# Performance work log

Measured on AMD Instinct MI355X. Metric: run time of the kernel, lower is better.

Reference implementation:

```python
import jax, jax.numpy as jnp
import numpy as np

BN_EPS = 1e-5

def conv2d(x, w, pad):
    return jax.lax.conv_general_dilated(x, w, (1, 1), [(pad, pad), (pad, pad)],
                                        dimension_numbers=('NCHW', 'OIHW', 'NCHW'))

def bn(x, g, b, m, v):
    # eval-mode batchnorm with running stats
    c = (None, slice(None), None, None)
    return g[c] * (x - m[c]) * jax.lax.rsqrt(v[c] + BN_EPS) + b[c]

def criss_cross_attention(x, wq, wk, wv, gamma):
    # x: (B, C, H, W); q/k have reduced dim d = C//8
    B, C, H, W = x.shape
    q = jnp.einsum('bchw,dc->bdhw', x, wq)
    k = jnp.einsum('bchw,dc->bdhw', x, wk)
    v = jnp.einsum('bchw,dc->bdhw', x, wv)
    # column (vertical) affinities: for each (h,w), keys at (k,w) -> (B,H,W,H)
    eH = jnp.einsum('bdhw,bdkw->bhwk', q, k)
    # -inf on the h==k diagonal (avoid counting the center pixel twice)
    eH = eH + jnp.where(jnp.eye(H, dtype=bool), -jnp.inf, 0.0)[None, :, None, :]
    # row (horizontal) affinities: keys at (h,k) -> (B,H,W,W)
    eW = jnp.einsum('bdhw,bdhk->bhwk', q, k)
    att = jax.nn.softmax(jnp.concatenate([eH, eW], axis=3), axis=3)  # (B,H,W,H+W)
    aH, aW = att[..., :H], att[..., H:]
    oH = jnp.einsum('bhwk,bdkw->bdhw', aH, v)
    oW = jnp.einsum('bhwk,bdhk->bdhw', aW, v)
    return gamma * (oH + oW) + x

def upsample_bilinear_align_corners(x, out_h, out_w):
    # torch nn.Upsample(mode='bilinear', align_corners=True)
    def interp(x, size, axis):
        n = x.shape[axis]
        pos = jnp.arange(size, dtype=x.dtype) * ((n - 1) / (size - 1))
        lo = jnp.floor(pos).astype(jnp.int32)
        hi = jnp.minimum(lo + 1, n - 1)
        w = pos - lo.astype(x.dtype)
        shp = [1] * x.ndim; shp[axis] = size
        w = w.reshape(shp)
        return jnp.take(x, lo, axis=axis) * (1 - w) + jnp.take(x, hi, axis=axis) * w
    x = interp(x, out_h, 2)
    return interp(x, out_w, 3)

def setup_inputs() -> dict:
    key = jax.random.key(0)
    ks = jax.random.split(key, 16)
    B, C, H, W = 2, 2048, 96, 96
    ic = C // 32          # inter_c = 64
    dq = ic // 8          # 8
    nc = 19
    s = 0.05
    return {
        'x': jax.random.normal(ks[0], (B, C, H, W), jnp.float32),
        'w_in': jax.random.normal(ks[1], (ic, C, 3, 3), jnp.float32) * s,
        'bn_in_g': jnp.ones((ic,), jnp.float32),
        'bn_in_b': jnp.zeros((ic,), jnp.float32),
        'bn_in_m': jax.random.normal(ks[2], (ic,), jnp.float32) * 0.1,
        'bn_in_v': jax.random.uniform(ks[3], (ic,), jnp.float32, 0.5, 1.5),
        'wq': jax.random.normal(ks[4], (dq, ic), jnp.float32) * s,
        'wk': jax.random.normal(ks[5], (dq, ic), jnp.float32) * s,
        'wv': jax.random.normal(ks[6], (ic, ic), jnp.float32) * s,
        'cca_gamma': jax.random.uniform(ks[7], (1,), jnp.float32, 0.2, 0.8),
        'w_out': jax.random.normal(ks[8], (ic, ic, 3, 3), jnp.float32) * s,
        'bn_out_g': jnp.ones((ic,), jnp.float32),
        'bn_out_b': jnp.zeros((ic,), jnp.float32),
        'bn_out_m': jax.random.normal(ks[9], (ic,), jnp.float32) * 0.1,
        'bn_out_v': jax.random.uniform(ks[10], (ic,), jnp.float32, 0.5, 1.5),
        'w_cls1': jax.random.normal(ks[11], (ic, C + ic, 3, 3), jnp.float32) * s,
        'bn_cls_g': jnp.ones((ic,), jnp.float32),
        'bn_cls_b': jnp.zeros((ic,), jnp.float32),
        'bn_cls_m': jax.random.normal(ks[12], (ic,), jnp.float32) * 0.1,
        'bn_cls_v': jax.random.uniform(ks[13], (ic,), jnp.float32, 0.5, 1.5),
        'w_cls2': jax.random.normal(ks[14], (nc, ic, 1, 1), jnp.float32) * s,
    }

def reference(x, w_in, bn_in_g, bn_in_b, bn_in_m, bn_in_v,
              wq, wk, wv, cca_gamma,
              w_out, bn_out_g, bn_out_b, bn_out_m, bn_out_v,
              w_cls1, bn_cls_g, bn_cls_b, bn_cls_m, bn_cls_v, w_cls2):
    RECURRENCE = 2
    out = jax.nn.relu(bn(conv2d(x, w_in, 1), bn_in_g, bn_in_b, bn_in_m, bn_in_v))
    for _ in range(RECURRENCE):
        out = criss_cross_attention(out, wq, wk, wv, cca_gamma)
    out = jax.nn.relu(bn(conv2d(out, w_out, 1), bn_out_g, bn_out_b, bn_out_m, bn_out_v))
    out = jnp.concatenate([x, out], axis=1)
    # cls_seg: conv -> BN (no relu) -> upsample x8 (bilinear, align_corners) -> 1x1 conv
    out = bn(conv2d(out, w_cls1, 1), bn_cls_g, bn_cls_b, bn_cls_m, bn_cls_v)
    H, W = out.shape[2], out.shape[3]
    out = upsample_bilinear_align_corners(out, H * 8, W * 8)
    out = conv2d(out, w_cls2, 0)
    return out
```

## Files before the change

### kernel.cpp

```cpp
#include <hip/hip_runtime.h>
#include <stdint.h>

#define HW 9216

typedef float f32x4 __attribute__((ext_vector_type(4)));
typedef short s16x8 __attribute__((ext_vector_type(8)));

#define PIN() asm volatile("" ::: "memory")
#define WAITV12() asm volatile("s_waitcnt vmcnt(12)" ::: "memory")

__device__ __forceinline__ unsigned short f2bf(float f){
  union { float fv; uint32_t u; } x; x.fv = f;
  uint32_t u = x.u;
  u += 0x7fffu + ((u >> 16) & 1u);
  return (unsigned short)(u >> 16);
}
__device__ __forceinline__ float bf2f(unsigned short s){
  union { uint32_t u; float fv; } x; x.u = ((uint32_t)s) << 16;
  return x.fv;
}

__device__ __forceinline__ void gload16(const void* g, void* l){
  __builtin_amdgcn_global_load_lds(
    (const __attribute__((address_space(1))) unsigned int*)g,
    (__attribute__((address_space(3))) unsigned int*)l, 16, 0, 0);
}

__global__ __launch_bounds__(256) void transp_pack_kernel(const float* __restrict__ x,
    unsigned short* __restrict__ xT,
    const float* __restrict__ w_in, const float* __restrict__ w_out,
    const float* __restrict__ w_cls1, unsigned short* __restrict__ WpIn,
    unsigned short* __restrict__ WpOut, unsigned short* __restrict__ WpCls,
    unsigned short* __restrict__ zp){
  __shared__ unsigned short tl[256 * 66];
  int blk = blockIdx.x;
  int tid = threadIdx.x;
  if (blk < 2304){
    int b = blk / 1152; int r = blk - b * 1152;
    int cchunk = r / 144, pxt = r - cchunk * 144;
    int c0 = cchunk * 256, px0 = pxt * 64;
    for (int e = tid; e < 4096; e += 256){
      int cc = e >> 4, pq = e & 15;
      float4 v4 = *(const float4*)(x + ((size_t)(b * 2048 + c0 + cc)) * HW + px0 + pq * 4);
      const float* vp = (const float*)&v4;
      #pragma unroll
      for (int j = 0; j < 4; j++) tl[cc * 66 + pq * 4 + j] = f2bf(vp[j]);
    }
    __syncthreads();
    for (int j = tid; j < 2048; j += 256){
      int px = j >> 5, oct = j & 31;
      s16x8 pk;
      #pragma unroll
      for (int t = 0; t < 8; t++) pk[t] = (short)tl[(oct * 8 + t) * 66 + px];
      *(s16x8*)(xT + ((size_t)(b * 9216 + px0 + px)) * 2048 + c0 + oct * 8) = pk;
    }
  } else {
    if (blk == 2304 && tid < 64) ((unsigned int*)zp)[tid] = 0u;
    const int N0 = 64 * 2048 * 9, N1 = 64 * 64 * 9, N2 = 64 * 2112 * 9;
    int total = N0 + N1 + N2;
    int nblk = gridDim.x - 2304;
    for (int i = (blk - 2304) * 256 + tid; i < total; i += nblk * 256){
      const float* w; unsigned short* Wp; int Cin; int idx;
      if (i < N0){ w = w_in; Wp = WpIn; Cin = 2048; idx = i; }
      else if (i < N0 + N1){ w = w_out; Wp = WpOut; Cin = 64; idx = i - N0; }
      else { w = w_cls1; Wp = WpCls; Cin = 2112; idx = i - N0 - N1; }
      int c = idx & 31; int r = idx >> 5; int o = r & 63; int r2 = r >> 6;
      int tap = r2 % 9; int ck = r2 / 9;
      Wp[idx] = f2bf(w[((size_t)o * Cin + ck * 32 + c) * 9 + tap]);
    }
  }
}

template<int T>
__device__ __forceinline__ void tapbody(const char* hb, s16x8 (&bs)[4], f32x4 (&acc)[4][4],
    const unsigned short* wbase, int gmax, int g0, int wv, int ln, int kg){
  constexpr int dy = T / 3, dx = T - dy * 3;
  #pragma unroll
  for (int mf = 0; mf < 4; mf++){
    int p = (wv * 4 + mf + dy) * 18 + (ln + dx);
    int aoff = p * 64 + ((kg ^ (p & 3)) << 4);
    s16x8 a = *(const s16x8*)(hb + aoff);
    #pragma unroll
    for (int nf = 0; nf < 4; nf++)
      acc[mf][nf] = __builtin_amdgcn_mfma_f32_16x16x32_bf16(a, bs[nf], acc[mf][nf], 0, 0, 0);
  }
  constexpr int dck = (T + 3) / 9, dt = (T + 3) % 9;
  if (g0 + T + 3 < gmax){
    const unsigned short* wb2 = wbase + dck * 18432 + dt * 2048;
    #pragma unroll
    for (int nf = 0; nf < 4; nf++) bs[nf] = *(const s16x8*)(wb2 + nf * 512);
  }
}

__global__ __launch_bounds__(256, 2) void conv_nhwc_kernel(
    const unsigned short* __restrict__ A0, int c0stride,
    const unsigned short* __restrict__ A1, int nck0,
    const unsigned short* __restrict__ Wp,
    unsigned short* __restrict__ sl, int nchunks,
    const unsigned short* __restrict__ zp){
  int mt = blockIdx.x;
  int b = mt / 36; int r = mt - b * 36;
  int h0 = (r / 6) * 16, w0 = (r % 6) * 16;
  int KS = gridDim.y, ks = blockIdx.y;
  int c0 = (nchunks * ks) / KS, c1 = (nchunks * (ks + 1)) / KS;
  int tid = threadIdx.x, lane = tid & 63, wv = tid >> 6;
  int ln = lane & 15, kg = lane >> 4;
  __shared__ char halo[2][24576];

  int pixb0[6], pixb1[6]; bool val[6];
  #pragma unroll
  for (int rr = 0; rr < 6; rr++){
    int i = tid + rr * 256;
    int p = i >> 2, q_lds = i & 3;
    int logq = q_lds ^ (p & 3);
    int hh = p / 18, ww = p - hh * 18;
    int h = h0 - 1 + hh, w = w0 - 1 + ww;
    bool v = (i < 1296) && ((unsigned)h < 96u) && ((unsigned)w < 96u);
    val[rr] = v;
    int pix = (b * 96 + h) * 96 + w;
    pixb0[rr] = v ? (pix * c0stride * 2 + logq * 16) : 0;
    pixb1[rr] = v ? (pix * 128 + logq * 16) : 0;
  }
  const char* a0B = (const char*)A0;
  const char* a1B = (const char*)A1;
  const char* zpB = (const char*)zp;

  auto stage = [&](char* ldsB, int ck){
    bool inA0 = (ck < nck0);
    int chb0 = ck * 64, chb1 = (ck - nck0) * 64;
    #pragma unroll
    for (int rr = 0; rr < 6; rr++){
      const char* src = zpB;
      if (val[rr]) src = inA0 ? (a0B + pixb0[rr] + chb0) : (a1B + pixb1[rr] + chb1);
      gload16(src, ldsB + (tid + rr * 256) * 16);
    }
  };

  f32x4 acc[4][4];
  #pragma unroll
  for (int i = 0; i < 4; i++)
    #pragma unroll
    for (int j = 0; j < 4; j++) acc[i][j] = (f32x4)(0.f);

  s16x8 bs0[4], bs1[4], bs2[4];
  int gmax = (c1 - c0) * 9;

  stage(&halo[0][0], c0);
  PIN();
  {
    const unsigned short* w0b = Wp + (size_t)c0 * 18432 + ln * 32 + kg * 8;
    #pragma unroll
    for (int nf = 0; nf < 4; nf++){
      bs0[nf] = *(const s16x8*)(w0b + 0 * 2048 + nf * 512);
      bs1[nf] = *(const s16x8*)(w0b + 1 * 2048 + nf * 512);
      bs2[nf] = *(const s16x8*)(w0b + 2 * 2048 + nf * 512);
    }
  }
  WAITV12();
  __builtin_amdgcn_s_barrier();

  for (int ck = c0; ck < c1; ck++){
    int cur = (ck - c0) & 1;
    if (ck + 1 < c1){ stage(&halo[cur ^ 1][0], ck + 1); PIN(); }
    const unsigned short* wbase = Wp + (size_t)ck * 18432 + ln * 32 + kg * 8;
    const char* hb = &halo[cur][0];
    int g0 = (ck - c0) * 9;
    tapbody<0>(hb, bs0, acc, wbase, gmax, g0, wv, ln, kg);
    tapbody<1>(hb, bs1, acc, wbase, gmax, g0, wv, ln, kg);
    tapbody<2>(hb, bs2, acc, wbase, gmax, g0, wv, ln, kg);
    tapbody<3>(hb, bs0, acc, wbase, gmax, g0, wv, ln, kg);
    tapbody<4>(hb, bs1, acc, wbase, gmax, g0, wv, ln, kg);
    tapbody<5>(hb, bs2, acc, wbase, gmax, g0, wv, ln, kg);
    tapbody<6>(hb, bs0, acc, wbase, gmax, g0, wv, ln, kg);
    tapbody<7>(hb, bs1, acc, wbase, gmax, g0, wv, ln, kg);
    tapbody<8>(hb, bs2, acc, wbase, gmax, g0, wv, ln, kg);
    if (ck + 1 < c1){
      WAITV12();
      __builtin_amdgcn_s_barrier();
    }
  }

  unsigned short* base = sl + ((size_t)(ks * 72 + mt)) * 16384;
  #pragma unroll
  for (int mf = 0; mf < 4; mf++)
    #pragma unroll
    for (int nf = 0; nf < 4; nf++){
      int o = nf * 16 + ln;
      #pragma unroll
      for (int rr = 0; rr < 4; rr++){
        int m = wv * 64 + mf * 16 + kg * 4 + rr;
        base[m * 64 + o] = f2bf(acc[mf][nf][rr]);
      }
    }
}

__global__ __launch_bounds__(256, 2) void conv_out_kernel(
    const unsigned short* __restrict__ A0,
    const unsigned short* __restrict__ Wp,
    const float* __restrict__ g, const float* __restrict__ bb,
    const float* __restrict__ mm, const float* __restrict__ vv,
    unsigned short* __restrict__ outT,
    const unsigned short* __restrict__ zp){
  int mt = blockIdx.x;
  int b = mt / 36; int r = mt - b * 36;
  int h0 = (r / 6) * 16, w0 = (r % 6) * 16;
  int tid = threadIdx.x, lane = tid & 63, wv = tid >> 6;
  int ln = lane & 15, kg = lane >> 4;
  __shared__ char halo[2][24576];

  int pixb0[6]; bool val[6];
  #pragma unroll
  for (int rr = 0; rr < 6; rr++){
    int i = tid + rr * 256;
    int p = i >> 2, q_lds = i & 3;
    int logq = q_lds ^ (p & 3);
    int hh = p / 18, ww = p - hh * 18;
    int h = h0 - 1 + hh, w = w0 - 1 + ww;
    bool v = (i < 1296) && ((unsigned)h < 96u) && ((unsigned)w < 96u);
    val[rr] = v;
    int pix = (b * 96 + h) * 96 + w;
    pixb0[rr] = v ? (pix * 128 + logq * 16) : 0;
  }
  const char* a0B = (const char*)A0;
  const char* zpB = (const char*)zp;

  auto stage = [&](char* ldsB, int ck){
    int chb0 = ck * 64;
    #pragma unroll
    for (int rr = 0; rr < 6; rr++){
      const char* src = val[rr] ? (a0B + pixb0[rr] + chb0) : zpB;
      gload16(src, ldsB + (tid + rr * 256) * 16);
    }
  };

  f32x4 acc[4][4];
  #pragma unroll
  for (int i = 0; i < 4; i++)
    #pragma unroll
    for (int j = 0; j < 4; j++) acc[i][j] = (f32x4)(0.f);

  s16x8 bs0[4], bs1[4], bs2[4];

  stage(&halo[0][0], 0);
  PIN();
  {
    const unsigned short* w0b = Wp + ln * 32 + kg * 8;
    #pragma unroll
    for (int nf = 0; nf < 4; nf++){
      bs0[nf] = *(const s16x8*)(w0b + 0 * 2048 + nf * 512);
      bs1[nf] = *(const s16x8*)(w0b + 1 * 2048 + nf * 512);
      bs2[nf] = *(const s16x8*)(w0b + 2 * 2048 + nf * 512);
    }
  }
  WAITV12();
  __builtin_amdgcn_s_barrier();

  for (int ck = 0; ck < 2; ck++){
    int cur = ck & 1;
    if (ck == 0){ stage(&halo[1][0], 1); PIN(); }
    const unsigned short* wbase = Wp + (size_t)ck * 18432 + ln * 32 + kg * 8;
    const char* hb = &halo[cur][0];
    int g0 = ck * 9;
    tapbody<0>(hb, bs0, acc, wbase, 18, g0, wv, ln, kg);
    tapbody<1>(hb, bs1, acc, wbase, 18, g0, wv, ln, kg);
    tapbody<2>(hb, bs2, acc, wbase, 18, g0, wv, ln, kg);
    tapbody<3>(hb, bs0, acc, wbase, 18, g0, wv, ln, kg);
    tapbody<4>(hb, bs1, acc, wbase, 18, g0, wv, ln, kg);
    tapbody<5>(hb, bs2, acc, wbase, 18, g0, wv, ln, kg);
    tapbody<6>(hb, bs0, acc, wbase, 18, g0, wv, ln, kg);
    tapbody<7>(hb, bs1, acc, wbase, 18, g0, wv, ln, kg);
    tapbody<8>(hb, bs2, acc, wbase, 18, g0, wv, ln, kg);
    if (ck == 0){
      WAITV12();
      __builtin_amdgcn_s_barrier();
    }
  }

  #pragma unroll
  for (int nf = 0; nf < 4; nf++){
    int o = nf * 16 + ln;
    float sc = g[o] * rsqrtf(vv[o] + 1e-5f);
    float mo = mm[o], bo = bb[o];
    #pragma unroll
    for (int mf = 0; mf < 4; mf++)
      #pragma unroll
      for (int rr = 0; rr < 4; rr++){
        int m = wv * 64 + mf * 16 + kg * 4 + rr;
        int h = h0 + (m >> 4), w = w0 + (m & 15);
        float valf = (acc[mf][nf][rr] - mo) * sc + bo;
        valf = fmaxf(valf, 0.f);
        outT[(((size_t)b * 96 + h) * 96 + w) * 64 + o] = f2bf(valf);
      }
  }
}

__global__ __launch_bounds__(256) void bn_reduce_kernel(const unsigned short* __restrict__ sl,
    int KS, const float* __restrict__ g, const float* __restrict__ bb,
    const float* __restrict__ mm, const float* __restrict__ vv, int relu,
    unsigned short* __restrict__ out, int do_proj,
    const float* __restrict__ wq, const float* __restrict__ wk, const float* __restrict__ wv,
    float* __restrict__ q, float* __restrict__ k, unsigned short* __restrict__ v){
  __shared__ float yl[4 * 65];
  __shared__ float wqL[8 * 65], wkL[8 * 65], wvL[64 * 65];
  int tid = threadIdx.x;
  if (do_proj){
    for (int i = tid; i < 512; i += 256){
      int d = i >> 6, c = i & 63;
      wqL[d * 65 + c] = wq[i]; wkL[d * 65 + c] = wk[i];
    }
    for (int i = tid; i < 4096; i += 256){
      int o = i >> 6, c = i & 63;
      wvL[o * 65 + c] = wv[i];
    }
  }
  int idx = blockIdx.x * 256 + tid;
  int mt = idx >> 14, e = idx & 16383;
  int m = e >> 6, o = e & 63;
  float s = 0.f;
  for (int ks = 0; ks < KS; ks++) s += bf2f(sl[((size_t)(ks * 72 + mt)) * 16384 + e]);
  float sc = g[o] * rsqrtf(vv[o] + 1e-5f);
  float valf = (s - mm[o]) * sc + bb[o];
  if (relu) valf = fmaxf(valf, 0.f);
  int b = mt / 36; int r = mt - b * 36;
  int h = (r / 6) * 16 + (m >> 4), w = (r % 6) * 16 + (m & 15);
  out[(((size_t)b * 96 + h) * 96 + w) * 64 + o] = f2bf(valf);
  if (do_proj){
    int px = tid >> 6;
    yl[px * 65 + o] = valf;
    __syncthreads();
    int m2 = ((blockIdx.x & 63) << 2) + px;
    int h2 = (r / 6) * 16 + (m2 >> 4), w2 = (r % 6) * 16 + (m2 & 15);
    size_t pix2 = ((size_t)b * 96 + h2) * 96 + w2;
    float va = 0.f;
    #pragma unroll 8
    for (int c = 0; c < 64; c++) va += wvL[o * 65 + c] * yl[px * 65 + c];
    v[pix2 * 64 + o] = f2bf(va);
    if (o < 16){
      const float* wsel = (o < 8) ? wqL : wkL;
      int d = o & 7;
      float qa = 0.f;
      #pragma unroll 8
      for (int c = 0; c < 64; c++) qa += wsel[d * 65 + c] * yl[px * 65 + c];
      if (o < 8) q[pix2 * 8 + d] = qa; else k[pix2 * 8 + d] = qa;
    }
  }
}

__global__ __launch_bounds__(256) void bn_reduce_cls_kernel(const unsigned short* __restrict__ sl,
    int KS, const float* __restrict__ g, const float* __restrict__ bb,
    const float* __restrict__ mm, const float* __restrict__ vv,
    const float* __restrict__ w2, float* __restrict__ t19){
  __shared__ float yl[4][64];
  __shared__ float w2L[19 * 64];
  int tid = threadIdx.x;
  for (int i = tid; i < 1216; i += 256) w2L[i] = w2[i];
  int idx = blockIdx.x * 256 + tid;
  int mt = idx >> 14, e = idx & 16383;
  int o = e & 63;
  float s = 0.f;
  for (int ks = 0; ks < KS; ks++) s += bf2f(sl[((size_t)(ks * 72 + mt)) * 16384 + e]);
  float sc = g[o] * rsqrtf(vv[o] + 1e-5f);
  float valf = (s - mm[o]) * sc + bb[o];
  yl[tid >> 6][o] = valf;
  __syncthreads();
  if (tid < 76){
    int mq = tid / 19, j = tid - mq * 19;
    float a = 0.f;
    #pragma unroll 8
    for (int c = 0; c < 64; c++) a += w2L[j * 64 + c] * yl[mq][c];
    int m = ((blockIdx.x & 63) << 2) + mq;
    int b = mt / 36; int r = mt - b * 36;
    int h = (r / 6) * 16 + (m >> 4), w = (r % 6) * 16 + (m & 15);
    t19[((size_t)(b * 19 + j)) * HW + h * 96 + w] = a;
  }
}

__global__ __launch_bounds__(256) void cca_proj_kernel(const unsigned short* __restrict__ xin,
    const float* __restrict__ wq, const float* __restrict__ wk, const float* __restrict__ wv,
    float* __restrict__ q, float* __restrict__ k, unsigned short* __restrict__ v){
  __shared__ float wqL[512], wkL[512], wvL[4096];
  int tid = threadIdx.x;
  for (int i = tid; i < 512; i += 256){ wqL[i] = wq[i]; wkL[i] = wk[i]; }
  for (int i = tid; i < 4096; i += 256) wvL[i] = wv[i];
  __syncthreads();
  int gid = blockIdx.x * 256 + tid;
  int gp = gid >> 1, half = gid & 1;
  unsigned short xv16[64];
  #pragma unroll
  for (int t = 0; t < 8; t++)
    *(s16x8*)(&xv16[t * 8]) = *(const s16x8*)(xin + (size_t)gp * 64 + t * 8);
  float qa[4], ka[4], va[32];
  #pragma unroll
  for (int d = 0; d < 4; d++){ qa[d] = 0.f; ka[d] = 0.f; }
  #pragma unroll
  for (int d = 0; d < 32; d++) va[d] = 0.f;
  int qo = half * 4, vo = half * 32;
  #pragma unroll 4
  for (int c = 0; c < 64; c++){
    float xv = bf2f(xv16[c]);
    #pragma unroll
    for (int d = 0; d < 4; d++){ qa[d] += wqL[(qo + d) * 64 + c] * xv; ka[d] += wkL[(qo + d) * 64 + c] * xv; }
    #pragma unroll
    for (int d = 0; d < 32; d++) va[d] += wvL[(vo + d) * 64 + c] * xv;
  }
  #pragma unroll
  for (int d = 0; d < 4; d++){ q[(size_t)gp * 8 + qo + d] = qa[d]; k[(size_t)gp * 8 + qo + d] = ka[d]; }
  #pragma unroll
  for (int t = 0; t < 4; t++){
    s16x8 pk;
    #pragma unroll
    for (int j = 0; j < 8; j++) pk[j] = (short)f2bf(va[t * 8 + j]);
    *(s16x8*)(v + (size_t)gp * 64 + vo + t * 8) = pk;
  }
}

__global__ __launch_bounds__(256, 2) void cca_rowSM_kernel(const float* __restrict__ qT,
    const float* __restrict__ kT, const unsigned short* __restrict__ vT,
    const unsigned short* __restrict__ xin, const float* __restrict__ gamma,
    float* __restrict__ ebuf, unsigned short* __restrict__ xout){
  int blk = blockIdx.x;
  int b = blk / 192; int r = blk - b * 192; int h = r >> 1, z = r & 1;
  __shared__ float qrL[48 * 12], krL[96 * 12];
  __shared__ float ewT[96 * 50];
  __shared__ float vLf[96 * 68];
  __shared__ float aWf[48 * 100];
  int tid = threadIdx.x;
  int lane = tid & 63, wvid = tid >> 6;
  size_t rowb = (size_t)(b * HW) + h * 96;
  const float* ebase = ebuf + rowb * 96;

  for (int i = tid; i < 384; i += 256){
    int wl = i >> 3, d = i & 7;
    qrL[wl * 12 + d] = qT[(rowb + z * 48 + wl) * 8 + d];
  }
  for (int i = tid; i < 768; i += 256){
    int wp = i >> 3, d = i & 7;
    krL[wp * 12 + d] = kT[(rowb + wp) * 8 + d];
  }
  for (int i = tid; i < 768; i += 256){
    int wp = i >> 3, oct = i & 7;
    s16x8 v8 = *(const s16x8*)(vT + (rowb + wp) * 64 + oct * 8);
    #pragma unroll
    for (int j = 0; j < 8; j++) vLf[wp * 68 + oct * 8 + j] = bf2f((unsigned short)v8[j]);
  }
  __syncthreads();
  {
    int wl0 = (tid & 15) * 3, kp0 = (tid >> 4) * 6;
    f32x4 q0[3], q1[3], k0[6], k1[6];
    #pragma unroll
    for (int i = 0; i < 3; i++){
      q0[i] = *(const f32x4*)&qrL[(wl0 + i) * 12];
      q1[i] = *(const f32x4*)&qrL[(wl0 + i) * 12 + 4];
    }
    #pragma unroll
    for (int j = 0; j < 6; j++){
      k0[j] = *(const f32x4*)&krL[(kp0 + j) * 12];
      k1[j] = *(const f32x4*)&krL[(kp0 + j) * 12 + 4];
    }
    #pragma unroll
    for (int j = 0; j < 6; j++)
      #pragma unroll
      for (int i = 0; i < 3; i++){
        float e = 0.f;
        #pragma unroll
        for (int d = 0; d < 4; d++) e += q0[i][d] * k0[j][d] + q1[i][d] * k1[j][d];
        ewT[(kp0 + j) * 50 + (wl0 + i)] = e;
      }
  }
  __syncthreads();
  #pragma unroll 2
  for (int t = 0; t < 12; t++){
    int wl = wvid + t * 4;
    int w = z * 48 + wl;
    f32x4 qa = *(const f32x4*)&qrL[wl * 12];
    f32x4 qb4 = *(const f32x4*)&qrL[wl * 12 + 4];
    const float* kc0 = kT + ((size_t)(b * HW) + (size_t)lane * 96 + w) * 8;
    f32x4 k0a = *(const f32x4*)kc0;
    f32x4 k0b = *(const f32x4*)(kc0 + 4);
    float x0 = 0.f;
    #pragma unroll
    for (int d = 0; d < 4; d++) x0 += qa[d] * k0a[d] + qb4[d] * k0b[d];
    if (lane == h) x0 = -1e30f;
    float x1;
    if (lane < 32){
      const float* kc1 = kT + ((size_t)(b * HW) + (size_t)(64 + lane) * 96 + w) * 8;
      f32x4 k1a = *(const f32x4*)kc1;
      f32x4 k1b = *(const f32x4*)(kc1 + 4);
      x1 = 0.f;
      #pragma unroll
      for (int d = 0; d < 4; d++) x1 += qa[d] * k1a[d] + qb4[d] * k1b[d];
      if (64 + lane == h) x1 = -1e30f;
    } else {
      x1 = ewT[(lane - 32) * 50 + wl];
    }
    float x2 = ewT[(lane + 32) * 50 + wl];
    float mx = fmaxf(x0, fmaxf(x1, x2));
    #pragma unroll
    for (int s = 32; s; s >>= 1) mx = fmaxf(mx, __shfl_xor(mx, s));
    float e0 = __expf(x0 - mx), e1 = __expf(x1 - mx), e2 = __expf(x2 - mx);
    float sm = e0 + e1 + e2;
    #pragma unroll
    for (int s = 32; s; s >>= 1) sm += __shfl_xor(sm, s);
    float inv = 1.f / sm;
    float* ebw = (float*)(ebase + (size_t)w * 96);
    ebw[lane] = e0 * inv;
    if (lane < 32) ebw[64 + lane] = e1 * inv;
    else           aWf[wl * 100 + (lane - 32)] = e1 * inv;
    aWf[wl * 100 + (lane + 32)] = e2 * inv;
  }
  __syncthreads();
  float gm = gamma[0];
  int d0 = (tid & 15) * 4, wl0 = (tid >> 4) * 3;
  f32x4 acc2[3];
  #pragma unroll
  for (int c = 0; c < 3; c++) acc2[c] = (f32x4)(0.f);
  for (int kp = 0; kp < 96; kp += 4){
    f32x4 a0 = *(const f32x4*)&aWf[(wl0 + 0) * 100 + kp];
    f32x4 a1 = *(const f32x4*)&aWf[(wl0 + 1) * 100 + kp];
    f32x4 a2 = *(const f32x4*)&aWf[(wl0 + 2) * 100 + kp];
    #pragma unroll
    for (int j = 0; j < 4; j++){
      f32x4 vv = *(const f32x4*)&vLf[(kp + j) * 68 + d0];
      acc2[0] += vv * a0[j];
      acc2[1] += vv * a1[j];
      acc2[2] += vv * a2[j];
    }
  }
  #pragma unroll
  for (int c = 0; c < 3; c++){
    size_t pix = rowb + z * 48 + wl0 + c;
    ushort4 xr = *(const ushort4*)&xin[pix * 64 + d0];
    ushort4 ov;
    ov.x = f2bf(bf2f(xr.x) + gm * acc2[c][0]);
    ov.y = f2bf(bf2f(xr.y) + gm * acc2[c][1]);
    ov.z = f2bf(bf2f(xr.z) + gm * acc2[c][2]);
    ov.w = f2bf(bf2f(xr.w) + gm * acc2[c][3]);
    *(ushort4*)&xout[pix * 64 + d0] = ov;
  }
}

__global__ __launch_bounds__(256, 2) void cca_colO_kernel(const unsigned short* __restrict__ vT,
    const float* __restrict__ gamma, const float* __restrict__ ebuf,
    const unsigned short* __restrict__ xpart, unsigned short* __restrict__ xout){
  int blk = blockIdx.x;
  int b = blk / 192; int r = blk - b * 192; int w = r >> 1, z = r & 1;
  __shared__ float vLf[96 * 68];
  __shared__ float aTf[48 * 100];
  int tid = threadIdx.x;
  for (int i = tid; i < 768; i += 256){
    int kp = i >> 3, oct = i & 7;
    s16x8 v8 = *(const s16x8*)(vT + ((size_t)(b * HW) + kp * 96 + w) * 64 + oct * 8);
    #pragma unroll
    for (int j = 0; j < 8; j++) vLf[kp * 68 + oct * 8 + j] = bf2f((unsigned short)v8[j]);
  }
  for (int i = tid; i < 4608; i += 256){
    int hl = i / 96, kp = i - hl * 96;
    aTf[hl * 100 + kp] = ebuf[(((size_t)b * 96 + z * 48 + hl) * 96 + w) * 96 + kp];
  }
  __syncthreads();
  float gm = gamma[0];
  int d0 = (tid & 15) * 4, hl0 = (tid >> 4) * 3;
  f32x4 acc2[3];
  #pragma unroll
  for (int c = 0; c < 3; c++) acc2[c] = (f32x4)(0.f);
  for (int kp = 0; kp < 96; kp += 4){
    f32x4 a0 = *(const f32x4*)&aTf[(hl0 + 0) * 100 + kp];
    f32x4 a1 = *(const f32x4*)&aTf[(hl0 + 1) * 100 + kp];
    f32x4 a2 = *(const f32x4*)&aTf[(hl0 + 2) * 100 + kp];
    #pragma unroll
    for (int j = 0; j < 4; j++){
      f32x4 vv = *(const f32x4*)&vLf[(kp + j) * 68 + d0];
      acc2[0] += vv * a0[j];
      acc2[1] += vv * a1[j];
      acc2[2] += vv * a2[j];
    }
  }
  #pragma unroll
  for (int c = 0; c < 3; c++){
    size_t pix = (size_t)(b * HW) + (z * 48 + hl0 + c) * 96 + w;
    ushort4 xr = *(const ushort4*)&xpart[pix * 64 + d0];
    ushort4 ov;
    ov.x = f2bf(bf2f(xr.x) + gm * acc2[c][0]);
    ov.y = f2bf(bf2f(xr.y) + gm * acc2[c][1]);
    ov.z = f2bf(bf2f(xr.z) + gm * acc2[c][2]);
    ov.w = f2bf(bf2f(xr.w) + gm * acc2[c][3]);
    *(ushort4*)&xout[pix * 64 + d0] = ov;
  }
}

__global__ void upsample_kernel(const float* __restrict__ t19, float* __restrict__ out){
  int gid = blockIdx.x * 256 + threadIdx.x;
  int xq = gid % 192; int t = gid / 192;
  int yy = t % 768; t /= 768;
  int o = t % 19; int b = t / 19;
  const float R = 95.0f / 767.0f;
  float ry = yy * R;
  int iy = (int)ry;
  float fy = ry - (float)iy;
  int iy1 = min(iy + 1, 95);
  const float* base = t19 + ((size_t)b * 19 + o) * HW;
  float4 res;
  float* rp = (float*)&res;
  #pragma unroll
  for (int j = 0; j < 4; j++){
    int xx = xq * 4 + j;
    float rx = xx * R;
    int ix = (int)rx; float fx = rx - (float)ix; int ix1 = min(ix + 1, 95);
    float v00 = base[iy * 96 + ix],  v01 = base[iy * 96 + ix1];
    float v10 = base[iy1 * 96 + ix], v11 = base[iy1 * 96 + ix1];
    rp[j] = (1.f - fy) * ((1.f - fx) * v00 + fx * v01) + fy * ((1.f - fx) * v10 + fx * v11);
  }
  *(float4*)(out + (((size_t)b * 19 + o) * 768 + yy) * 768 + xq * 4) = res;
}

extern "C" void kernel_launch(void* const* d_in, const int* in_sizes, int n_in,
                              void* d_out, int out_size, void* d_ws, size_t ws_size,
                              hipStream_t stream){
  const float* x       = (const float*)d_in[0];
  const float* w_in    = (const float*)d_in[1];
  const float* bn_in_g = (const float*)d_in[2];
  const float* bn_in_b = (const float*)d_in[3];
  const float* bn_in_m = (const float*)d_in[4];
  const float* bn_in_v = (const float*)d_in[5];
  const float* wq      = (const float*)d_in[6];
  const float* wk      = (const float*)d_in[7];
  const float* wv      = (const float*)d_in[8];
  const float* gamma   = (const float*)d_in[9];
  const float* w_out   = (const float*)d_in[10];
  const float* bn_o_g  = (const float*)d_in[11];
  const float* bn_o_b  = (const float*)d_in[12];
  const float* bn_o_m  = (const float*)d_in[13];
  const float* bn_o_v  = (const float*)d_in[14];
  const float* w_cls1  = (const float*)d_in[15];
  const float* bn_c_g  = (const float*)d_in[16];
  const float* bn_c_b  = (const float*)d_in[17];
  const float* bn_c_m  = (const float*)d_in[18];
  const float* bn_c_v  = (const float*)d_in[19];
  const float* w_cls2  = (const float*)d_in[20];
  float* out = (float*)d_out;

  char* ws = (char*)d_ws;
  size_t off = 0;
  auto alloc = [&](size_t bytes) -> void* {
    void* p = ws + off; off += (bytes + 255) & ~(size_t)255; return p;
  };
  const int KS = 12;
  const size_t NHWCb = (size_t)2 * HW * 64 * 2;
  unsigned short* xT   = (unsigned short*)alloc((size_t)2 * HW * 2048 * 2);
  unsigned short* sl   = (unsigned short*)alloc((size_t)KS * 72 * 16384 * 2);
  float* ebuf = (float*)sl;
  unsigned short* xattA = (unsigned short*)alloc(NHWCb);
  unsigned short* xattB = (unsigned short*)alloc(NHWCb);
  unsigned short* Ptmp  = (unsigned short*)alloc(NHWCb);
  unsigned short* attT  = (unsigned short*)alloc(NHWCb);
  unsigned short* midT  = (unsigned short*)alloc(NHWCb);
  float* qb    = (float*)alloc((size_t)2 * HW * 8 * 4);
  float* kb    = (float*)alloc((size_t)2 * HW * 8 * 4);
  unsigned short* vb = (unsigned short*)alloc(NHWCb);
  float* t19   = (float*)alloc((size_t)2 * 19 * HW * 4);
  unsigned short* WpIn  = (unsigned short*)alloc((size_t)64 * 2048 * 9 * 2);
  unsigned short* WpOut = (unsigned short*)alloc((size_t)64 * 64 * 9 * 2);
  unsigned short* WpCls = (unsigned short*)alloc((size_t)64 * 2112 * 9 * 2);
  unsigned short* zp    = (unsigned short*)alloc(256);
  (void)ws_size; (void)in_sizes; (void)n_in; (void)out_size;

  transp_pack_kernel<<<2304 + 512, 256, 0, stream>>>(x, xT, w_in, w_out, w_cls1,
      WpIn, WpOut, WpCls, zp);

  conv_nhwc_kernel<<<dim3(72, KS), 256, 0, stream>>>(xT, 2048, nullptr, 64, WpIn, sl, 64, zp);
  bn_reduce_kernel<<<4608, 256, 0, stream>>>(sl, KS, bn_in_g, bn_in_b, bn_in_m, bn_in_v, 1,
      xattA, 1, wq, wk, wv, qb, kb, vb);

  cca_rowSM_kernel<<<384, 256, 0, stream>>>(qb, kb, vb, xattA, gamma, ebuf, Ptmp);
  cca_colO_kernel<<<384, 256, 0, stream>>>(vb, gamma, ebuf, Ptmp, xattB);
  cca_proj_kernel<<<144, 256, 0, stream>>>(xattB, wq, wk, wv, qb, kb, vb);
  cca_rowSM_kernel<<<384, 256, 0, stream>>>(qb, kb, vb, xattB, gamma, ebuf, Ptmp);
  cca_colO_kernel<<<384, 256, 0, stream>>>(vb, gamma, ebuf, Ptmp, attT);

  conv_out_kernel<<<72, 256, 0, stream>>>(attT, WpOut, bn_o_g, bn_o_b, bn_o_m, bn_o_v, midT, zp);

  conv_nhwc_kernel<<<dim3(72, KS), 256, 0, stream>>>(xT, 2048, midT, 64, WpCls, sl, 66, zp);
  bn_reduce_cls_kernel<<<4608, 256, 0, stream>>>(sl, KS, bn_c_g, bn_c_b, bn_c_m, bn_c_v, w_cls2, t19);

  upsample_kernel<<<21888, 256, 0, stream>>>(t19, out);
}
```

Measured before the change: 388.0 us.

## Split conv tile across eight waves and pad transpose LDS stride to 65

The main 3x3 conv kernel now launches 512 threads per block, with 8 waves each computing 2 row fragments instead of 4 waves computing 4. This is meant to raise latency hiding. Halo staging is spread over the larger thread count, and tapbody is templated on the fragment count so conv_out keeps its 4-fragment layout. Separately, the transpose LDS tile row stride changes from 66 to 65 shorts to alter its bank mapping. The trade-off is that each wave reuses its loaded weight fragments over fewer MFMAs, so weight-load traffic per MFMA rises. The tighter register budget implied by launch_bounds(512,4) could also cause spills.

```diff
diff --git a/kernel.cpp b/kernel.cpp
--- a/kernel.cpp
+++ b/kernel.cpp
@@ -32,7 +32,7 @@
     const float* __restrict__ w_cls1, unsigned short* __restrict__ WpIn,
     unsigned short* __restrict__ WpOut, unsigned short* __restrict__ WpCls,
     unsigned short* __restrict__ zp){
-  __shared__ unsigned short tl[256 * 66];
+  __shared__ unsigned short tl[256 * 65];
   int blk = blockIdx.x;
   int tid = threadIdx.x;
   if (blk < 2304){
@@ -44,14 +44,14 @@
       float4 v4 = *(const float4*)(x + ((size_t)(b * 2048 + c0 + cc)) * HW + px0 + pq * 4);
       const float* vp = (const float*)&v4;
       #pragma unroll
-      for (int j = 0; j < 4; j++) tl[cc * 66 + pq * 4 + j] = f2bf(vp[j]);
+      for (int j = 0; j < 4; j++) tl[cc * 65 + pq * 4 + j] = f2bf(vp[j]);
     }
     __syncthreads();
     for (int j = tid; j < 2048; j += 256){
       int px = j >> 5, oct = j & 31;
       s16x8 pk;
       #pragma unroll
-      for (int t = 0; t < 8; t++) pk[t] = (short)tl[(oct * 8 + t) * 66 + px];
+      for (int t = 0; t < 8; t++) pk[t] = (short)tl[(oct * 8 + t) * 65 + px];
       *(s16x8*)(xT + ((size_t)(b * 9216 + px0 + px)) * 2048 + c0 + oct * 8) = pk;
     }
   } else {
@@ -71,13 +71,13 @@
   }
 }
 
-template<int T>
-__device__ __forceinline__ void tapbody(const char* hb, s16x8 (&bs)[4], f32x4 (&acc)[4][4],
-    const unsigned short* wbase, int gmax, int g0, int wv, int ln, int kg){
+template<int T, int NMF>
+__device__ __forceinline__ void tapbody(const char* hb, s16x8 (&bs)[4], f32x4 (&acc)[NMF][4],
+    const unsigned short* wbase, int gmax, int g0, int rowbase, int ln, int kg){
   constexpr int dy = T / 3, dx = T - dy * 3;
   #pragma unroll
-  for (int mf = 0; mf < 4; mf++){
-    int p = (wv * 4 + mf + dy) * 18 + (ln + dx);
+  for (int mf = 0; mf < NMF; mf++){
+    int p = (rowbase + mf + dy) * 18 + (ln + dx);
     int aoff = p * 64 + ((kg ^ (p & 3)) << 4);
     s16x8 a = *(const s16x8*)(hb + aoff);
     #pragma unroll
@@ -92,7 +92,7 @@
   }
 }
 
-__global__ __launch_bounds__(256, 2) void conv_nhwc_kernel(
+__global__ __launch_bounds__(512, 4) void conv_nhwc_kernel(
     const unsigned short* __restrict__ A0, int c0stride,
     const unsigned short* __restrict__ A1, int nck0,
     const unsigned short* __restrict__ Wp,
@@ -107,10 +107,10 @@
   int ln = lane & 15, kg = lane >> 4;
   __shared__ char halo[2][24576];
 
-  int pixb0[6], pixb1[6]; bool val[6];
-  #pragma unroll
-  for (int rr = 0; rr < 6; rr++){
-    int i = tid + rr * 256;
+  int pixb0[3], pixb1[3]; bool val[3];
+  #pragma unroll
+  for (int rr = 0; rr < 3; rr++){
+    int i = tid + rr * 512;
     int p = i >> 2, q_lds = i & 3;
     int logq = q_lds ^ (p & 3);
     int hh = p / 18, ww = p - hh * 18;
@@ -129,21 +129,22 @@
     bool inA0 = (ck < nck0);
     int chb0 = ck * 64, chb1 = (ck - nck0) * 64;
     #pragma unroll
-    for (int rr = 0; rr < 6; rr++){
+    for (int rr = 0; rr < 3; rr++){
       const char* src = zpB;
       if (val[rr]) src = inA0 ? (a0B + pixb0[rr] + chb0) : (a1B + pixb1[rr] + chb1);
-      gload16(src, ldsB + (tid + rr * 256) * 16);
+      gload16(src, ldsB + (tid + rr * 512) * 16);
     }
   };
 
-  f32x4 acc[4][4];
-  #pragma unroll
-  for (int i = 0; i < 4; i++)
+  f32x4 acc[2][4];
+  #pragma unroll
+  for (int i = 0; i < 2; i++)
     #pragma unroll
     for (int j = 0; j < 4; j++) acc[i][j] = (f32x4)(0.f);
 
   s16x8 bs0[4], bs1[4], bs2[4];
   int gmax = (c1 - c0) * 9;
+  int rowbase = wv * 2;
 
   stage(&halo[0][0], c0);
   PIN();
@@ -165,15 +166,15 @@
     const unsigned short* wbase = Wp + (size_t)ck * 18432 + ln * 32 + kg * 8;
     const char* hb = &halo[cur][0];
     int g0 = (ck - c0) * 9;
-    tapbody<0>(hb, bs0, acc, wbase, gmax, g0, wv, ln, kg);
-    tapbody<1>(hb, bs1, acc, wbase, gmax, g0, wv, ln, kg);
-    tapbody<2>(hb, bs2, acc, wbase, gmax, g0, wv, ln, kg);
-    tapbody<3>(hb, bs0, acc, wbase, gmax, g0, wv, ln, kg);
-    tapbody<4>(hb, bs1, acc, wbase, gmax, g0, wv, ln, kg);
-    tapbody<5>(hb, bs2, acc, wbase, gmax, g0, wv, ln, kg);
-    tapbody<6>(hb, bs0, acc, wbase, gmax, g0, wv, ln, kg);
-    tapbody<7>(hb, bs1, acc, wbase, gmax, g0, wv, ln, kg);
-    tapbody<8>(hb, bs2, acc, wbase, gmax, g0, wv, ln, kg);
+    tapbody<0,2>(hb, bs0, acc, wbase, gmax, g0, rowbase, ln, kg);
+    tapbody<1,2>(hb, bs1, acc, wbase, gmax, g0, rowbase, ln, kg);
+    tapbody<2,2>(hb, bs2, acc, wbase, gmax, g0, rowbase, ln, kg);
+    tapbody<3,2>(hb, bs0, acc, wbase, gmax, g0, rowbase, ln, kg);
+    tapbody<4,2>(hb, bs1, acc, wbase, gmax, g0, rowbase, ln, kg);
+    tapbody<5,2>(hb, bs2, acc, wbase, gmax, g0, rowbase, ln, kg);
+    tapbody<6,2>(hb, bs0, acc, wbase, gmax, g0, rowbase, ln, kg);
+    tapbody<7,2>(hb, bs1, acc, wbase, gmax, g0, rowbase, ln, kg);
+    tapbody<8,2>(hb, bs2, acc, wbase, gmax, g0, rowbase, ln, kg);
     if (ck + 1 < c1){
       WAITV12();
       __builtin_amdgcn_s_barrier();
@@ -182,13 +183,13 @@
 
   unsigned short* base = sl + ((size_t)(ks * 72 + mt)) * 16384;
   #pragma unroll
-  for (int mf = 0; mf < 4; mf++)
+  for (int mf = 0; mf < 2; mf++)
     #pragma unroll
     for (int nf = 0; nf < 4; nf++){
       int o = nf * 16 + ln;
       #pragma unroll
       for (int rr = 0; rr < 4; rr++){
-        int m = wv * 64 + mf * 16 + kg * 4 + rr;
+        int m = (rowbase + mf) * 16 + kg * 4 + rr;
         base[m * 64 + o] = f2bf(acc[mf][nf][rr]);
       }
     }
@@ -240,6 +241,7 @@
     for (int j = 0; j < 4; j++) acc[i][j] = (f32x4)(0.f);
 
   s16x8 bs0[4], bs1[4], bs2[4];
+  int rowbase = wv * 4;
 
   stage(&halo[0][0], 0);
   PIN();
@@ -261,15 +263,15 @@
     const unsigned short* wbase = Wp + (size_t)ck * 18432 + ln * 32 + kg * 8;
     const char* hb = &halo[cur][0];
     int g0 = ck * 9;
-    tapbody<0>(hb, bs0, acc, wbase, 18, g0, wv, ln, kg);
-    tapbody<1>(hb, bs1, acc, wbase, 18, g0, wv, ln, kg);
-    tapbody<2>(hb, bs2, acc, wbase, 18, g0, wv, ln, kg);
-    tapbody<3>(hb, bs0, acc, wbase, 18, g0, wv, ln, kg);
-    tapbody<4>(hb, bs1, acc, wbase, 18, g0, wv, ln, kg);
-    tapbody<5>(hb, bs2, acc, wbase, 18, g0, wv, ln, kg);
-    tapbody<6>(hb, bs0, acc, wbase, 18, g0, wv, ln, kg);
-    tapbody<7>(hb, bs1, acc, wbase, 18, g0, wv, ln, kg);
-    tapbody<8>(hb, bs2, acc, wbase, 18, g0, wv, ln, kg);
+    tapbody<0,4>(hb, bs0, acc, wbase, 18, g0, rowbase, ln, kg);
+    tapbody<1,4>(hb, bs1, acc, wbase, 18, g0, rowbase, ln, kg);
+    tapbody<2,4>(hb, bs2, acc, wbase, 18, g0, rowbase, ln, kg);
+    tapbody<3,4>(hb, bs0, acc, wbase, 18, g0, rowbase, ln, kg);
+    tapbody<4,4>(hb, bs1, acc, wbase, 18, g0, rowbase, ln, kg);
+    tapbody<5,4>(hb, bs2, acc, wbase, 18, g0, rowbase, ln, kg);
+    tapbody<6,4>(hb, bs0, acc, wbase, 18, g0, rowbase, ln, kg);
+    tapbody<7,4>(hb, bs1, acc, wbase, 18, g0, rowbase, ln, kg);
+    tapbody<8,4>(hb, bs2, acc, wbase, 18, g0, rowbase, ln, kg);
     if (ck == 0){
       WAITV12();
       __builtin_amdgcn_s_barrier();
@@ -285,7 +287,7 @@
     for (int mf = 0; mf < 4; mf++)
       #pragma unroll
       for (int rr = 0; rr < 4; rr++){
-        int m = wv * 64 + mf * 16 + kg * 4 + rr;
+        int m = (rowbase + mf) * 16 + kg * 4 + rr;
         int h = h0 + (m >> 4), w = w0 + (m & 15);
         float valf = (acc[mf][nf][rr] - mo) * sc + bo;
         valf = fmaxf(valf, 0.f);
@@ -667,7 +669,7 @@
   transp_pack_kernel<<<2304 + 512, 256, 0, stream>>>(x, xT, w_in, w_out, w_cls1,
       WpIn, WpOut, WpCls, zp);
 
-  conv_nhwc_kernel<<<dim3(72, KS), 256, 0, stream>>>(xT, 2048, nullptr, 64, WpIn, sl, 64, zp);
+  conv_nhwc_kernel<<<dim3(72, KS), 512, 0, stream>>>(xT, 2048, nullptr, 64, WpIn, sl, 64, zp);
   bn_reduce_kernel<<<4608, 256, 0, stream>>>(sl, KS, bn_in_g, bn_in_b, bn_in_m, bn_in_v, 1,
       xattA, 1, wq, wk, wv, qb, kb, vb);
 
@@ -679,7 +681,7 @@
 
   conv_out_kernel<<<72, 256, 0, stream>>>(attT, WpOut, bn_o_g, bn_o_b, bn_o_m, bn_o_v, midT, zp);
 
-  conv_nhwc_kernel<<<dim3(72, KS), 256, 0, stream>>>(xT, 2048, midT, 64, WpCls, sl, 66, zp);
+  conv_nhwc_kernel<<<dim3(72, KS), 512, 0, stream>>>(xT, 2048, midT, 64, WpCls, sl, 66, zp);
   bn_reduce_cls_kernel<<<4608, 256, 0, stream>>>(sl, KS, bn_c_g, bn_c_b, bn_c_m, bn_c_v, w_cls2, t19);
 
   upsample_kernel<<<21888, 256, 0, stream>>>(t19, out);
```

Result: slower. 497.7 us (+28.3%).
